# Performance work log

Measured on AMD Instinct MI355X. Metric: run time of the kernel, lower is better.

Reference implementation:

```python
import jax, jax.numpy as jnp
import numpy as np

DIM = 512
NUM_HEADS = 8
HEAD_DIM = DIM // NUM_HEADS
MAX_SIZE = 128


def setup_inputs() -> dict:
    key = jax.random.key(0)
    ks = jax.random.split(key, 13)
    B, C, H, W = 4, DIM, 128, 128
    inp = {
        "x": jax.random.normal(ks[0], (B, C, H, W), jnp.float32),
        "q_w": jax.random.normal(ks[1], (DIM, DIM), jnp.float32) * 0.02,
        "q_b": jax.random.normal(ks[2], (DIM,), jnp.float32) * 0.02,
        "k_w": jax.random.normal(ks[3], (DIM, DIM), jnp.float32) * 0.02,
        "k_b": jax.random.normal(ks[4], (DIM,), jnp.float32) * 0.02,
        "v_w": jax.random.normal(ks[5], (DIM, DIM), jnp.float32) * 0.02,
        "v_b": jax.random.normal(ks[6], (DIM,), jnp.float32) * 0.02,
        "o_w": jax.random.normal(ks[7], (DIM, DIM), jnp.float32) * 0.02,
        "o_b": jax.random.normal(ks[8], (DIM,), jnp.float32) * 0.02,
        "pos_q": jax.random.normal(ks[9], (1, NUM_HEADS, MAX_SIZE, HEAD_DIM), jnp.float32),
        "pos_k": jax.random.normal(ks[10], (1, NUM_HEADS, MAX_SIZE, HEAD_DIM), jnp.float32),
        "pos_v": jax.random.normal(ks[11], (1, NUM_HEADS, MAX_SIZE, HEAD_DIM), jnp.float32),
        "g_q": jnp.ones((1,), jnp.float32),
        "g_k": jnp.ones((1,), jnp.float32),
        "g_v1": jnp.ones((1,), jnp.float32),
        "g_v2": jnp.ones((1,), jnp.float32),
    }
    return inp


def _gated_axial_attn(x, q_w, q_b, k_w, k_b, v_w, v_b, o_w, o_b,
                      pos_q, pos_k, pos_v, g_q, g_k, g_v1, g_v2):
    B, C, H, W = x.shape
    nh, hd = NUM_HEADS, C // NUM_HEADS
    scale = hd ** (-0.5)
    # axis='width': attend along W for each (B,H) row
    xf = jnp.transpose(x, (0, 2, 3, 1)).reshape(B * H, W, C)  # (BH, W, C)

    def proj(w, b):
        y = xf @ w.T + b                       # (BH, W, C)
        return jnp.transpose(y.reshape(B * H, W, nh, hd), (0, 2, 1, 3))  # (BH, nh, W, hd)

    q = proj(q_w, q_b)
    k = proj(k_w, k_b)
    v = proj(v_w, v_b)

    pq = pos_q[0, :, :W, :]  # (nh, W, hd)
    pk = pos_k[0, :, :W, :]
    pv = pos_v[0, :, :W, :]

    # scores[i,j] = q_i.k_j + g_q * q_i.pq_j + g_k * pk_i.k_j, all scaled
    scores = jnp.einsum('bnid,bnjd->bnij', q, k)
    scores = scores + g_q[0] * jnp.einsum('bnid,njd->bnij', q, pq)
    scores = scores + g_k[0] * jnp.einsum('nid,bnjd->bnij', pk, k)
    attn = jax.nn.softmax(scores * scale, axis=-1)  # (BH, nh, W, W)

    vmix = g_v1[0] * v + g_v2[0] * pv[None]        # (BH, nh, W, hd)
    out = jnp.einsum('bnij,bnjd->bnid', attn, vmix)
    out = jnp.transpose(out, (0, 2, 1, 3)).reshape(B * H, W, C)
    out = out @ o_w.T + o_b
    return jnp.transpose(out.reshape(B, H, W, C), (0, 3, 1, 2))  # (B, C, H, W)


def reference(x, q_w, q_b, k_w, k_b, v_w, v_b, o_w, o_b,
              pos_q, pos_k, pos_v, g_q, g_k, g_v1, g_v2):
    return _gated_axial_attn(x, q_w, q_b, k_w, k_b, v_w, v_b, o_w, o_b,
                             pos_q, pos_k, pos_v, g_q, g_k, g_v1, g_v2)
```

## Files before the change

### kernel.cpp

```cpp
#include <hip/hip_runtime.h>

typedef __bf16 bf16;
typedef __attribute__((ext_vector_type(8))) __bf16 bf16x8;
typedef __attribute__((ext_vector_type(4))) __bf16 bf16x4;
typedef __attribute__((ext_vector_type(4))) float fvec4;

#define MFMA16(a, b, c) __builtin_amdgcn_mfma_f32_16x16x32_bf16(a, b, c, 0, 0, 0)

__device__ __forceinline__ void glds16(const bf16* g, bf16* l) {
  __builtin_amdgcn_global_load_lds(
      (const __attribute__((address_space(1))) void*)g,
      (__attribute__((address_space(3))) void*)l, 16, 0, 0);
}

__device__ inline fvec4 zero4() { fvec4 z = {0.f, 0.f, 0.f, 0.f}; return z; }

#define PREP_ELEMS 1245184

__global__ __launch_bounds__(512) void prep_kernel(
    const float* __restrict__ qw, const float* __restrict__ kw,
    const float* __restrict__ vw, const float* __restrict__ ow,
    const float* __restrict__ pq, const float* __restrict__ pk,
    const float* __restrict__ pv, bf16* __restrict__ dst)
{
  int i = (blockIdx.x * 512 + threadIdx.x) * 4;
  const float* s;
  if      (i < 262144)  s = qw + i;
  else if (i < 524288)  s = kw + (i - 262144);
  else if (i < 786432)  s = vw + (i - 524288);
  else if (i < 1048576) s = ow + (i - 786432);
  else if (i < 1114112) s = pq + (i - 1048576);
  else if (i < 1179648) s = pk + (i - 1114112);
  else                  s = pv + (i - 1179648);
  fvec4 v = *(const fvec4*)s;
  bf16x4 o = { (bf16)v[0], (bf16)v[1], (bf16)v[2], (bf16)v[3] };
  *(bf16x4*)(dst + i) = o;
}

__global__ __launch_bounds__(256) void xpose_kernel(
    const float* __restrict__ x, bf16* __restrict__ xt, int bh0)
{
  __shared__ float Xs[64 * 133];
  const int cb = blockIdx.x, lb = blockIdx.y;
  const int bh = bh0 + lb, b = bh >> 7, h = bh & 127;
  const int t = threadIdx.x;
  const float* xb = x + (size_t)b * 8388608 + (size_t)(cb * 64) * 16384 + h * 128;
  #pragma unroll
  for (int it = 0; it < 8; ++it) {
    int idx = it * 256 + t;
    int c = idx >> 5, w4 = (idx & 31) << 2;
    fvec4 v = *(const fvec4*)(xb + (size_t)c * 16384 + w4);
    #pragma unroll
    for (int j = 0; j < 4; ++j) Xs[c * 133 + w4 + j] = v[j];
  }
  __syncthreads();
  const int c0 = (t & 7) * 8, wsub = t >> 3;
  #pragma unroll
  for (int wb = 0; wb < 4; ++wb) {
    int w = wb * 32 + wsub;
    bf16x8 o;
    #pragma unroll
    for (int i = 0; i < 8; ++i) o[i] = (bf16)Xs[(c0 + i) * 133 + w];
    *(bf16x8*)(xt + ((size_t)lb * 128 + w) * 512 + cb * 64 + c0) = o;
  }
}

__global__ __launch_bounds__(512, 4) void qkvattn_kernel(
    const bf16* __restrict__ xt, const bf16* __restrict__ wqkv,
    const float* __restrict__ q_b, const float* __restrict__ k_b,
    const float* __restrict__ v_b, const bf16* __restrict__ posb,
    const float* __restrict__ g_q, const float* __restrict__ g_k,
    const float* __restrict__ g_v1, const float* __restrict__ g_v2,
    bf16* __restrict__ ao)
{
  __shared__ bf16 SM[40960];
  bf16* Qs = SM;
  bf16* KP = SM + 8192;
  bf16* Vt = SM;

  const int nwg = gridDim.x;
  int wg = blockIdx.x;
  wg = (wg & 7) * (nwg >> 3) + (wg >> 3);
  const int lb = wg >> 3, n = wg & 7;

  const int t = threadIdx.x;
  const int wv = t >> 6, lane = t & 63;
  const int lr = lane & 15, lg = lane >> 4;
  const int srow = lane >> 3, c16 = lane & 7;
  const int wm2 = wv >> 1, wn2 = wv & 1;

  fvec4 acc[2][6];
  #pragma unroll
  for (int i = 0; i < 2; ++i)
    #pragma unroll
    for (int j = 0; j < 6; ++j) acc[i][j] = zero4();

  const bf16* asrc[2];
  const bf16* bsrc[3];
  #pragma unroll
  for (int j = 0; j < 2; ++j) {
    int seg = wv * 2 + j;
    int row = seg * 8 + srow;
    int cs = c16 ^ (row & 7);
    asrc[j] = xt + (size_t)(lb * 128 + row) * 512 + cs * 8;
  }
  #pragma unroll
  for (int j = 0; j < 3; ++j) {
    int seg = wv * 3 + j;
    int row = seg * 8 + srow;
    int grow = ((row >> 6) << 9) + (n << 6) + (row & 63);
    int cs = c16 ^ (row & 7);
    bsrc[j] = wqkv + (size_t)grow * 512 + cs * 8;
  }

  #pragma unroll
  for (int j = 0; j < 2; ++j) glds16(asrc[j], SM + (wv * 2 + j) * 512);
  #pragma unroll
  for (int j = 0; j < 3; ++j) glds16(bsrc[j], SM + 8192 + (wv * 3 + j) * 512);

  int cur = 0;
  for (int k0 = 0; k0 < 512; k0 += 64) {
    __syncthreads();
    if (k0 < 448) {
      bf16* Ad = SM + (cur ^ 1) * 20480;
      bf16* Bd = Ad + 8192;
      #pragma unroll
      for (int j = 0; j < 2; ++j) glds16(asrc[j] + k0 + 64, Ad + (wv * 2 + j) * 512);
      #pragma unroll
      for (int j = 0; j < 3; ++j) glds16(bsrc[j] + k0 + 64, Bd + (wv * 3 + j) * 512);
    }
    const bf16* Ab = SM + cur * 20480;
    const bf16* Bb = Ab + 8192;
    #pragma unroll
    for (int kc = 0; kc < 2; ++kc) {
      bf16x8 af[2], bfv[6];
      #pragma unroll
      for (int mt = 0; mt < 2; ++mt) {
        int row = wm2 * 32 + mt * 16 + lr;
        int cs = (kc * 4 + lg) ^ (row & 7);
        af[mt] = *(const bf16x8*)(Ab + row * 64 + cs * 8);
      }
      #pragma unroll
      for (int nt = 0; nt < 6; ++nt) {
        int row = wn2 * 96 + nt * 16 + lr;
        int cs = (kc * 4 + lg) ^ (row & 7);
        bfv[nt] = *(const bf16x8*)(Bb + row * 64 + cs * 8);
      }
      #pragma unroll
      for (int mt = 0; mt < 2; ++mt)
        #pragma unroll
        for (int nt = 0; nt < 6; ++nt)
          acc[mt][nt] = MFMA16(af[mt], bfv[nt], acc[mt][nt]);
    }
    cur ^= 1;
  }
  __syncthreads();

  const float gq = g_q[0], gk = g_k[0], gv1 = g_v1[0], gv2 = g_v2[0];
  const bf16* pqb = posb + (size_t)n * 8192;
  const bf16* pkb = posb + 65536 + (size_t)n * 8192;
  const bf16* pvb = posb + 131072 + (size_t)n * 8192;

  #pragma unroll
  for (int mt = 0; mt < 2; ++mt) {
    #pragma unroll
    for (int nt = 0; nt < 6; ++nt) {
      int gc = wn2 * 96 + nt * 16 + lr;
      int sec = gc >> 6;
      int d = gc & 63;
      int rb = wm2 * 32 + mt * 16 + lg * 4;
      if (sec == 0) {
        float bq = q_b[n * 64 + d];
        #pragma unroll
        for (int r = 0; r < 4; ++r) {
          int row = rb + r;
          Qs[row * 64 + (((d >> 3) ^ (row & 7)) << 3) + (d & 7)] =
              (bf16)(acc[mt][nt][r] + bq);
        }
      } else if (sec == 1) {
        float bk = k_b[n * 64 + d];
        #pragma unroll
        for (int r = 0; r < 4; ++r) {
          int row = rb + r;
          float kv = acc[mt][nt][r] + bk;
          float pqv = (float)pqb[row * 64 + d];
          KP[row * 128 + (((d >> 3) ^ (row & 7)) << 3) + (d & 7)] =
              (bf16)(kv + gq * pqv);
          int d2 = 64 + d;
          KP[row * 128 + (((d2 >> 3) ^ (row & 7)) << 3) + (d2 & 7)] = (bf16)kv;
        }
      }
    }
  }
  __syncthreads();

  const int i0 = wv * 16;
  fvec4 s[8];
  #pragma unroll
  for (int i = 0; i < 8; ++i) s[i] = zero4();
  #pragma unroll
  for (int kc = 0; kc < 4; ++kc) {
    bf16x8 af;
    if (kc < 2) {
      int row = i0 + lr;
      int cs = (kc * 4 + lg) ^ (row & 7);
      af = *(const bf16x8*)(Qs + row * 64 + cs * 8);
    } else {
      bf16x8 raw = *(const bf16x8*)(pkb + (i0 + lr) * 64 + (kc - 2) * 32 + lg * 8);
      #pragma unroll
      for (int i = 0; i < 8; ++i) af[i] = (bf16)(gk * (float)raw[i]);
    }
    #pragma unroll
    for (int jt = 0; jt < 8; ++jt) {
      int row = jt * 16 + lr;
      int cs = (kc * 4 + lg) ^ (row & 7);
      bf16x8 bfr = *(const bf16x8*)(KP + row * 128 + cs * 8);
      s[jt] = MFMA16(af, bfr, s[jt]);
    }
  }

  const float scale = 0.125f;
  float inv[4];
  #pragma unroll
  for (int r = 0; r < 4; ++r) {
    float m = -1e30f;
    #pragma unroll
    for (int jt = 0; jt < 8; ++jt) m = fmaxf(m, s[jt][r]);
    #pragma unroll
    for (int off = 1; off < 16; off <<= 1) m = fmaxf(m, __shfl_xor(m, off));
    float sm = 0.f;
    #pragma unroll
    for (int jt = 0; jt < 8; ++jt) {
      float e = __expf((s[jt][r] - m) * scale);
      s[jt][r] = e;
      sm += e;
    }
    #pragma unroll
    for (int off = 1; off < 16; off <<= 1) sm += __shfl_xor(sm, off);
    inv[r] = 1.f / sm;
  }
  __syncthreads();

  #pragma unroll
  for (int r = 0; r < 4; ++r) {
    int i = i0 + lg * 4 + r;
    #pragma unroll
    for (int jt = 0; jt < 8; ++jt) {
      int j = jt * 16 + lr;
      KP[i * 128 + (((j >> 3) ^ (i & 7)) << 3) + (j & 7)] =
          (bf16)(s[jt][r] * inv[r]);
    }
  }
  if (wn2 == 1) {
    #pragma unroll
    for (int mt = 0; mt < 2; ++mt) {
      #pragma unroll
      for (int nt = 2; nt < 6; ++nt) {
        int d = nt * 16 - 32 + lr;
        float bv = v_b[n * 64 + d];
        #pragma unroll
        for (int r = 0; r < 4; ++r) {
          int j = wm2 * 32 + mt * 16 + lg * 4 + r;
          float vv = gv1 * (acc[mt][nt][r] + bv) + gv2 * (float)pvb[j * 64 + d];
          Vt[d * 128 + (((j >> 3) ^ (d & 7)) << 3) + (j & 7)] = (bf16)vv;
        }
      }
    }
  }
  __syncthreads();

  fvec4 o[4];
  #pragma unroll
  for (int i = 0; i < 4; ++i) o[i] = zero4();
  #pragma unroll
  for (int kc = 0; kc < 4; ++kc) {
    int prow = i0 + lr;
    int pcs = (kc * 4 + lg) ^ (prow & 7);
    bf16x8 af = *(const bf16x8*)(KP + prow * 128 + pcs * 8);
    #pragma unroll
    for (int dt = 0; dt < 4; ++dt) {
      int vr = dt * 16 + lr;
      int vcs = (kc * 4 + lg) ^ (vr & 7);
      bf16x8 bfr = *(const bf16x8*)(Vt + vr * 128 + vcs * 8);
      o[dt] = MFMA16(af, bfr, o[dt]);
    }
  }
  #pragma unroll
  for (int dt = 0; dt < 4; ++dt) {
    #pragma unroll
    for (int r = 0; r < 4; ++r) {
      int i = i0 + lg * 4 + r;
      ao[((size_t)lb * 128 + i) * 512 + n * 64 + dt * 16 + lr] = (bf16)o[dt][r];
    }
  }
}

__global__ __launch_bounds__(256, 3) void oproj_kernel(
    const bf16* __restrict__ ao, const bf16* __restrict__ wo,
    const float* __restrict__ o_b, float* __restrict__ out, int bh0)
{
  __shared__ bf16 As[128 * 64];
  __shared__ bf16 Bs[128 * 64];
  const int nwg = gridDim.x;
  int wg = blockIdx.x;
  if ((nwg & 7) == 0) wg = (wg & 7) * (nwg >> 3) + (wg >> 3);
  const int ct4 = wg & 3;
  const int lb = wg >> 2;
  const int bh = bh0 + lb, b = bh >> 7, h = bh & 127;
  const int t = threadIdx.x;
  const int wv = t >> 6, lane = t & 63;
  const int lr = lane & 15, lg = lane >> 4;
  const int wm = wv >> 1, wn = wv & 1;
  const int srow = lane >> 3, c16 = lane & 7;

  fvec4 acc[4][4];
  #pragma unroll
  for (int i = 0; i < 4; ++i)
    #pragma unroll
    for (int j = 0; j < 4; ++j) acc[i][j] = zero4();

  for (int k0 = 0; k0 < 512; k0 += 64) {
    __syncthreads();
    #pragma unroll
    for (int j = 0; j < 4; ++j) {
      int seg = wv * 4 + j;
      int row = seg * 8 + srow;
      int cs = c16 ^ (row & 7);
      glds16(wo + (size_t)(ct4 * 128 + row) * 512 + k0 + cs * 8, As + seg * 512);
      glds16(ao + ((size_t)lb * 128 + row) * 512 + k0 + cs * 8, Bs + seg * 512);
    }
    __syncthreads();
    #pragma unroll
    for (int kc = 0; kc < 2; ++kc) {
      bf16x8 af[4], bfv[4];
      #pragma unroll
      for (int mt = 0; mt < 4; ++mt) {
        int row = wm * 64 + mt * 16 + lr;
        int cs = (kc * 4 + lg) ^ (row & 7);
        af[mt] = *(const bf16x8*)(As + row * 64 + cs * 8);
      }
      #pragma unroll
      for (int nt = 0; nt < 4; ++nt) {
        int row = wn * 64 + nt * 16 + lr;
        int cs = (kc * 4 + lg) ^ (row & 7);
        bfv[nt] = *(const bf16x8*)(Bs + row * 64 + cs * 8);
      }
      #pragma unroll
      for (int mt = 0; mt < 4; ++mt)
        #pragma unroll
        for (int nt = 0; nt < 4; ++nt)
          acc[mt][nt] = MFMA16(af[mt], bfv[nt], acc[mt][nt]);
    }
  }
  #pragma unroll
  for (int mt = 0; mt < 4; ++mt) {
    #pragma unroll
    for (int r = 0; r < 4; ++r) {
      int co = ct4 * 128 + wm * 64 + mt * 16 + lg * 4 + r;
      float bv = o_b[co];
      size_t ob = ((size_t)(b * 512 + co) * 128 + h) * 128;
      #pragma unroll
      for (int nt = 0; nt < 4; ++nt) {
        int w = wn * 64 + nt * 16 + lr;
        out[ob + w] = acc[mt][nt][r] + bv;
      }
    }
  }
}

extern "C" void kernel_launch(void* const* d_in, const int* in_sizes, int n_in,
                              void* d_out, int out_size, void* d_ws, size_t ws_size,
                              hipStream_t stream) {
  const float* x    = (const float*)d_in[0];
  const float* q_w  = (const float*)d_in[1];
  const float* q_b  = (const float*)d_in[2];
  const float* k_w  = (const float*)d_in[3];
  const float* k_b  = (const float*)d_in[4];
  const float* v_w  = (const float*)d_in[5];
  const float* v_b  = (const float*)d_in[6];
  const float* o_w  = (const float*)d_in[7];
  const float* o_b  = (const float*)d_in[8];
  const float* pos_q = (const float*)d_in[9];
  const float* pos_k = (const float*)d_in[10];
  const float* pos_v = (const float*)d_in[11];
  const float* g_q  = (const float*)d_in[12];
  const float* g_k  = (const float*)d_in[13];
  const float* g_v1 = (const float*)d_in[14];
  const float* g_v2 = (const float*)d_in[15];
  float* out = (float*)d_out;

  bf16* prep = (bf16*)d_ws;
  bf16* wqkv = prep;
  bf16* wo   = prep + 786432;
  bf16* posb = prep + 1048576;

  bf16* rest = prep + PREP_ELEMS;
  size_t avail = (ws_size > (size_t)PREP_ELEMS * 2) ? ws_size - (size_t)PREP_ELEMS * 2 : 0;
  const size_t per_bh = (size_t)(65536 + 65536) * sizeof(bf16);
  int nbh = (int)(avail / per_bh);
  if (nbh > 512) nbh = 512;
  if (nbh < 1) nbh = 1;

  bf16* xt = rest;
  bf16* ao = xt + (size_t)nbh * 65536;

  prep_kernel<<<608, 512, 0, stream>>>(q_w, k_w, v_w, o_w, pos_q, pos_k, pos_v, prep);

  for (int bh0 = 0; bh0 < 512; bh0 += nbh) {
    int cur = (512 - bh0 < nbh) ? (512 - bh0) : nbh;
    xpose_kernel<<<dim3(8, cur), 256, 0, stream>>>(x, xt, bh0);
    qkvattn_kernel<<<cur * 8, 512, 0, stream>>>(xt, wqkv, q_b, k_b, v_b, posb,
                                                g_q, g_k, g_v1, g_v2, ao);
    oproj_kernel<<<cur * 4, 256, 0, stream>>>(ao, wo, o_b, out, bh0);
  }
}
```

Before: 494.9 us.

## Single-buffer QKV GEMM LDS and fold gate scalars into prepped pos tables

Drops the double-buffered LDS staging in the QKV projection loop in favour of a single buffer with load-then-sync each k-step. Shared memory shrinks from 80KB to 48KB and the launch bound rises from 4 to 6 blocks per CU, aiming for higher occupancy. Gate scalars g_q, g_k and g_v2 are now folded into the bf16 positional tables in the prep kernel, which removes per-element multiplies in the attention kernel. The cost is that global-to-LDS loads no longer overlap with MFMA work, leaving more latency for the extra resident blocks to hide.

```diff
diff --git a/kernel.cpp b/kernel.cpp
--- a/kernel.cpp
+++ b/kernel.cpp
@@ -21,19 +21,23 @@
     const float* __restrict__ qw, const float* __restrict__ kw,
     const float* __restrict__ vw, const float* __restrict__ ow,
     const float* __restrict__ pq, const float* __restrict__ pk,
-    const float* __restrict__ pv, bf16* __restrict__ dst)
+    const float* __restrict__ pv,
+    const float* __restrict__ g_q, const float* __restrict__ g_k,
+    const float* __restrict__ g_v2, bf16* __restrict__ dst)
 {
   int i = (blockIdx.x * 512 + threadIdx.x) * 4;
   const float* s;
+  float sc = 1.f;
   if      (i < 262144)  s = qw + i;
   else if (i < 524288)  s = kw + (i - 262144);
   else if (i < 786432)  s = vw + (i - 524288);
   else if (i < 1048576) s = ow + (i - 786432);
-  else if (i < 1114112) s = pq + (i - 1048576);
-  else if (i < 1179648) s = pk + (i - 1114112);
-  else                  s = pv + (i - 1179648);
+  else if (i < 1114112) { s = pq + (i - 1048576); sc = g_q[0]; }
+  else if (i < 1179648) { s = pk + (i - 1114112); sc = g_k[0]; }
+  else                  { s = pv + (i - 1179648); sc = g_v2[0]; }
   fvec4 v = *(const fvec4*)s;
-  bf16x4 o = { (bf16)v[0], (bf16)v[1], (bf16)v[2], (bf16)v[3] };
+  bf16x4 o = { (bf16)(v[0] * sc), (bf16)(v[1] * sc),
+               (bf16)(v[2] * sc), (bf16)(v[3] * sc) };
   *(bf16x4*)(dst + i) = o;
 }
 
@@ -65,15 +69,13 @@
   }
 }
 
-__global__ __launch_bounds__(512, 4) void qkvattn_kernel(
+__global__ __launch_bounds__(512, 6) void qkvattn_kernel(
     const bf16* __restrict__ xt, const bf16* __restrict__ wqkv,
     const float* __restrict__ q_b, const float* __restrict__ k_b,
     const float* __restrict__ v_b, const bf16* __restrict__ posb,
-    const float* __restrict__ g_q, const float* __restrict__ g_k,
-    const float* __restrict__ g_v1, const float* __restrict__ g_v2,
-    bf16* __restrict__ ao)
+    const float* __restrict__ g_v1, bf16* __restrict__ ao)
 {
-  __shared__ bf16 SM[40960];
+  __shared__ bf16 SM[24576];
   bf16* Qs = SM;
   bf16* KP = SM + 8192;
   bf16* Vt = SM;
@@ -113,24 +115,13 @@
     bsrc[j] = wqkv + (size_t)grow * 512 + cs * 8;
   }
 
-  #pragma unroll
-  for (int j = 0; j < 2; ++j) glds16(asrc[j], SM + (wv * 2 + j) * 512);
-  #pragma unroll
-  for (int j = 0; j < 3; ++j) glds16(bsrc[j], SM + 8192 + (wv * 3 + j) * 512);
-
-  int cur = 0;
   for (int k0 = 0; k0 < 512; k0 += 64) {
     __syncthreads();
-    if (k0 < 448) {
-      bf16* Ad = SM + (cur ^ 1) * 20480;
-      bf16* Bd = Ad + 8192;
-      #pragma unroll
-      for (int j = 0; j < 2; ++j) glds16(asrc[j] + k0 + 64, Ad + (wv * 2 + j) * 512);
-      #pragma unroll
-      for (int j = 0; j < 3; ++j) glds16(bsrc[j] + k0 + 64, Bd + (wv * 3 + j) * 512);
-    }
-    const bf16* Ab = SM + cur * 20480;
-    const bf16* Bb = Ab + 8192;
+    #pragma unroll
+    for (int j = 0; j < 2; ++j) glds16(asrc[j] + k0, SM + (wv * 2 + j) * 512);
+    #pragma unroll
+    for (int j = 0; j < 3; ++j) glds16(bsrc[j] + k0, SM + 8192 + (wv * 3 + j) * 512);
+    __syncthreads();
     #pragma unroll
     for (int kc = 0; kc < 2; ++kc) {
       bf16x8 af[2], bfv[6];
@@ -138,13 +129,13 @@
       for (int mt = 0; mt < 2; ++mt) {
         int row = wm2 * 32 + mt * 16 + lr;
         int cs = (kc * 4 + lg) ^ (row & 7);
-        af[mt] = *(const bf16x8*)(Ab + row * 64 + cs * 8);
+        af[mt] = *(const bf16x8*)(SM + row * 64 + cs * 8);
       }
       #pragma unroll
       for (int nt = 0; nt < 6; ++nt) {
         int row = wn2 * 96 + nt * 16 + lr;
         int cs = (kc * 4 + lg) ^ (row & 7);
-        bfv[nt] = *(const bf16x8*)(Bb + row * 64 + cs * 8);
+        bfv[nt] = *(const bf16x8*)(SM + 8192 + row * 64 + cs * 8);
       }
       #pragma unroll
       for (int mt = 0; mt < 2; ++mt)
@@ -152,11 +143,10 @@
         for (int nt = 0; nt < 6; ++nt)
           acc[mt][nt] = MFMA16(af[mt], bfv[nt], acc[mt][nt]);
     }
-    cur ^= 1;
   }
   __syncthreads();
 
-  const float gq = g_q[0], gk = g_k[0], gv1 = g_v1[0], gv2 = g_v2[0];
+  const float gv1 = g_v1[0];
   const bf16* pqb = posb + (size_t)n * 8192;
   const bf16* pkb = posb + 65536 + (size_t)n * 8192;
   const bf16* pvb = posb + 131072 + (size_t)n * 8192;
@@ -183,9 +173,8 @@
         for (int r = 0; r < 4; ++r) {
           int row = rb + r;
           float kv = acc[mt][nt][r] + bk;
-          float pqv = (float)pqb[row * 64 + d];
           KP[row * 128 + (((d >> 3) ^ (row & 7)) << 3) + (d & 7)] =
-              (bf16)(kv + gq * pqv);
+              (bf16)(kv + (float)pqb[row * 64 + d]);
           int d2 = 64 + d;
           KP[row * 128 + (((d2 >> 3) ^ (row & 7)) << 3) + (d2 & 7)] = (bf16)kv;
         }
@@ -206,9 +195,7 @@
       int cs = (kc * 4 + lg) ^ (row & 7);
       af = *(const bf16x8*)(Qs + row * 64 + cs * 8);
     } else {
-      bf16x8 raw = *(const bf16x8*)(pkb + (i0 + lr) * 64 + (kc - 2) * 32 + lg * 8);
-      #pragma unroll
-      for (int i = 0; i < 8; ++i) af[i] = (bf16)(gk * (float)raw[i]);
+      af = *(const bf16x8*)(pkb + (i0 + lr) * 64 + (kc - 2) * 32 + lg * 8);
     }
     #pragma unroll
     for (int jt = 0; jt < 8; ++jt) {
@@ -261,7 +248,7 @@
         #pragma unroll
         for (int r = 0; r < 4; ++r) {
           int j = wm2 * 32 + mt * 16 + lg * 4 + r;
-          float vv = gv1 * (acc[mt][nt][r] + bv) + gv2 * (float)pvb[j * 64 + d];
+          float vv = gv1 * (acc[mt][nt][r] + bv) + (float)pvb[j * 64 + d];
           Vt[d * 128 + (((j >> 3) ^ (d & 7)) << 3) + (j & 7)] = (bf16)vv;
         }
       }
@@ -404,13 +391,14 @@
   bf16* xt = rest;
   bf16* ao = xt + (size_t)nbh * 65536;
 
-  prep_kernel<<<608, 512, 0, stream>>>(q_w, k_w, v_w, o_w, pos_q, pos_k, pos_v, prep);
+  prep_kernel<<<608, 512, 0, stream>>>(q_w, k_w, v_w, o_w, pos_q, pos_k, pos_v,
+                                       g_q, g_k, g_v2, prep);
 
   for (int bh0 = 0; bh0 < 512; bh0 += nbh) {
     int cur = (512 - bh0 < nbh) ? (512 - bh0) : nbh;
     xpose_kernel<<<dim3(8, cur), 256, 0, stream>>>(x, xt, bh0);
     qkvattn_kernel<<<cur * 8, 512, 0, stream>>>(xt, wqkv, q_b, k_b, v_b, posb,
-                                                g_q, g_k, g_v1, g_v2, ao);
+                                                g_v1, ao);
     oproj_kernel<<<cur * 4, 256, 0, stream>>>(ao, wo, o_b, out, bh0);
   }
 }
```

After: 694.2 us. 40.3% more time.
